# Optimization experiments

Hardware: AMD Instinct MI355X
Metric: run time of the kernel (lower is better)

Reference implementation:

```python
import jax, jax.numpy as jnp
import numpy as np

B_SZ = 2; L = 512; D_MODEL = 1024
D_STATE = 128; HEADDIM = 64; NGROUPS = 1
D_INNER = 2048; D_SSM = 2048
NHEADS = D_SSM // HEADDIM          # 32
HPG = NHEADS // NGROUPS            # heads per group
HALF = D_STATE // 2
D_IN_PROJ = D_INNER + D_SSM + 2 * NGROUPS * D_STATE + NHEADS + NHEADS + NHEADS * HALF  # 6464
EPS = 1e-5

def _rms(v, w):
    return v * jax.lax.rsqrt(jnp.mean(v * v, axis=-1, keepdims=True) + EPS) * w

def _rope(v, c, s):
    v1, v2 = v[..., :HALF], v[..., HALF:]
    return jnp.concatenate([v1 * c - v2 * s, v2 * c + v1 * s], axis=-1)

def setup_inputs() -> dict:
    key = jax.random.key(0)
    ks = jax.random.split(key, 3)
    rng = np.random.default_rng(0)
    # dt_bias init per module: inverse-softplus of dt ~ LogUniform(dt_min, dt_max)
    dt = np.exp(rng.random(NHEADS) * (np.log(0.1) - np.log(0.001)) + np.log(0.001))
    dt = np.maximum(dt, 1e-4)
    dt_bias = (dt + np.log(-np.expm1(-dt))).astype(np.float32)
    A_log = np.log(rng.uniform(1.0, 16.0, NHEADS)).astype(np.float32)
    return {
        'u': jax.random.normal(ks[0], (B_SZ, L, D_MODEL), jnp.float32),
        'W_in': jax.random.normal(ks[1], (D_MODEL, D_IN_PROJ), jnp.float32) / np.sqrt(D_MODEL),
        'W_out': jax.random.normal(ks[2], (D_INNER, D_MODEL), jnp.float32) / np.sqrt(D_INNER),
        'dt_bias': jnp.asarray(dt_bias),
        'A_log': jnp.asarray(A_log),
        'D': jnp.ones((NHEADS,), jnp.float32),
        'B_bias': jnp.ones((NGROUPS * D_STATE,), jnp.float32),
        'C_bias': jnp.ones((NGROUPS * D_STATE,), jnp.float32),
        'B_norm_w': jnp.ones((D_STATE,), jnp.float32),
        'C_norm_w': jnp.ones((D_STATE,), jnp.float32),
        'norm_w': jnp.ones((D_SSM,), jnp.float32),
    }

def reference(u, W_in, W_out, dt_bias, A_log, D, B_bias, C_bias, B_norm_w, C_norm_w, norm_w):
    b, l, _ = u.shape
    zxbcdt = u @ W_in  # (b, l, d_in_proj)
    s0 = D_INNER; s1 = s0 + D_SSM
    s2 = s1 + NGROUPS * D_STATE; s3 = s2 + NGROUPS * D_STATE
    s4 = s3 + NHEADS; s5 = s4 + NHEADS
    z = zxbcdt[..., :s0]
    x = zxbcdt[..., s0:s1]
    Bv = zxbcdt[..., s1:s2]
    Cv = zxbcdt[..., s2:s3]
    dt_raw = zxbcdt[..., s3:s4]
    lam_raw = zxbcdt[..., s4:s5]
    theta = zxbcdt[..., s5:]
    # BC bias + QK RMSNorm
    Bg = _rms((Bv + B_bias).reshape(b, l, NGROUPS, D_STATE), B_norm_w)
    Cg = _rms((Cv + C_bias).reshape(b, l, NGROUPS, D_STATE), C_norm_w)
    # data-dependent RoPE with cumulative angles, averaged over heads per group
    cum = jnp.cumsum(theta.reshape(b, l, NHEADS, HALF), axis=1)
    cos = jnp.cos(cum).reshape(b, l, NGROUPS, HPG, HALF).mean(3)
    sin = jnp.sin(cum).reshape(b, l, NGROUPS, HPG, HALF).mean(3)
    Bg = _rope(Bg, cos, sin)
    Cg = _rope(Cg, cos, sin)
    # discretization
    dt = jax.nn.softplus(dt_raw + dt_bias)          # (b, l, nheads)
    dA = jnp.exp(dt * (-jnp.exp(A_log)))            # (b, l, nheads)
    x = jax.nn.silu(x).reshape(b, l, NHEADS, HEADDIM)
    # trapezoidal blending of x and B with previous step
    lam = jax.nn.sigmoid(lam_raw)                   # (b, l, nheads)
    x_prev = jnp.pad(x[:, :-1], ((0, 0), (1, 0), (0, 0), (0, 0)))
    x_eff = lam[..., None] * x + (1.0 - lam[..., None]) * x_prev
    B_prev = jnp.pad(Bg[:, :-1], ((0, 0), (1, 0), (0, 0), (0, 0)))
    lam_g = lam.reshape(b, l, NGROUPS, HPG).mean(-1)[..., None]
    B_eff = lam_g * Bg + (1.0 - lam_g) * B_prev
    # selective scan over time
    xs = jnp.moveaxis(x_eff.reshape(b, l, NGROUPS, HPG, HEADDIM), 1, 0)
    dAs = jnp.moveaxis(dA.reshape(b, l, NGROUPS, HPG), 1, 0)
    dts = jnp.moveaxis(dt.reshape(b, l, NGROUPS, HPG), 1, 0)
    Bs = jnp.moveaxis(B_eff, 1, 0)
    Cs = jnp.moveaxis(Cg, 1, 0)
    def step(h, inp):
        dA_t, dt_t, x_t, B_t, C_t = inp
        # h: (b, g, hpg, headdim, d_state)
        h = dA_t[..., None, None] * h + (dt_t[..., None] * x_t)[..., None] * B_t[:, :, None, None, :]
        y_t = jnp.einsum('bgnpd,bgd->bgnp', h, C_t)
        return h, y_t
    h0 = jnp.zeros((b, NGROUPS, HPG, HEADDIM, D_STATE), u.dtype)
    _, ys = jax.lax.scan(step, h0, (dAs, dts, xs, Bs, Cs))
    y = jnp.moveaxis(ys, 0, 1).reshape(b, l, NHEADS, HEADDIM) + D[None, None, :, None] * x_eff
    # gated RMSNorm (norm after gate), then output projection
    y = y.reshape(b, l, D_SSM) * jax.nn.silu(z)
    y = y * jax.lax.rsqrt(jnp.mean(y * y, axis=-1, keepdims=True) + EPS) * norm_w
    return y @ W_out
```

## Files before the change

kernel.cpp:

```cpp
#include <hip/hip_runtime.h>
#include <hip/hip_bf16.h>
#include <cstdint>

#define TOK 1024
#define LSEQ 512
#define DMODEL 1024
#define DPROJ 6464
#define DPROJP 6528
#define DSSM 2048
#define NHEADS 32
#define HEADDIM 64
#define DSTATE 128
#define NCH 8
#define CL 64

typedef __attribute__((ext_vector_type(4))) float f32x4;
typedef _Float16 f16;
typedef __attribute__((ext_vector_type(8))) _Float16 f16x8;
typedef __attribute__((ext_vector_type(4))) _Float16 f16x4;
typedef __attribute__((ext_vector_type(8))) ushort u16x8;

__device__ __forceinline__ float silu_f(float x){
  return x*__builtin_amdgcn_rcpf(1.f+__expf(-x));
}

__device__ __forceinline__ void gload16(const void* g, void* l){
  __builtin_amdgcn_global_load_lds(
      (const __attribute__((address_space(1))) unsigned int*)g,
      (__attribute__((address_space(3))) unsigned int*)l, 16, 0, 0);
}

__global__ __launch_bounds__(256) void prep_kernel(
    const float* __restrict__ W_in, const float* __restrict__ W_out,
    const float* __restrict__ u,
    f16* __restrict__ WT, f16* __restrict__ WoT, f16* __restrict__ uhf)
{
  int b = blockIdx.x;
  if (b < 6528 + 2048){
    __shared__ float tile[32][33];
    const float* W; f16* T; int K, N, bx, by;
    if (b < 6528){ W = W_in;  T = WT;  K = DMODEL; N = DPROJ;  bx = b % 204;      by = b / 204; }
    else         { int ib = b - 6528; W = W_out; T = WoT; K = DSSM; N = DMODEL; bx = ib & 31; by = ib >> 5; }
    int tx = threadIdx.x & 31, ty = threadIdx.x >> 5;
    int n = bx*32 + tx;
    #pragma unroll
    for (int i=0;i<4;i++){
      int k = by*32 + ty + i*8;
      tile[ty+i*8][tx] = (n < N) ? W[(size_t)k*N + n] : 0.f;
    }
    __syncthreads();
    #pragma unroll
    for (int i=0;i<4;i++){
      int nn = bx*32 + ty + i*8;
      int kk = by*32 + tx;
      T[(size_t)nn*K + kk] = (f16)tile[tx][ty+i*8];
    }
  } else {
    int i = (b - 8576)*256 + threadIdx.x;
    f32x4 v = ((const f32x4*)u)[i];
    f16x4 h;
    #pragma unroll
    for (int j=0;j<4;j++) h[j] = (f16)v[j];
    *(f16x4*)&uhf[(size_t)i*4] = h;
  }
}

template<bool HOUT>
__global__ __launch_bounds__(512) void gemmh_kernel(
    const f16* __restrict__ A, const f16* __restrict__ B,
    void* __restrict__ Cv, int K, int kLen, int ldc, int nbn, int chunk)
{
  __shared__ ushort sA[2][8192], sB[2][8192];
  int bid = blockIdx.x;
  int newL = (bid & 7)*chunk + (bid >> 3);
  int bm = newL & 7;
  int pan = newL >> 3;
  int bn = pan % nbn;
  int z  = pan / nbn;
  int k0 = z * kLen;
  size_t zoff = (size_t)z * 1024 * ldc;

  int tid = threadIdx.x;
  int wid = tid >> 6, lane = tid & 63;
  int wr = wid >> 2, wc = wid & 3;
  int fr = lane & 15, kq = lane >> 4;
  f32x4 acc[4][2] = {};

  int srow = tid & 127;
  int skg  = (tid >> 7) & 3;
  const f16* gA = A + (size_t)(bm*128+srow)*K + k0 + skg*8;
  const f16* gB = B + (size_t)(bn*128+srow)*K + k0 + skg*8;

  int rA = kq*1024 + (wr*64 + fr)*8;
  int rB = kq*1024 + (wc*32 + fr)*8;
  int NK = kLen >> 6;

#define STAGE(buf, kk) { \
    const f16* pa = gA + (kk)*64; \
    const f16* pb = gB + (kk)*64; \
    gload16(pa,      &sA[buf][tid*8]); \
    gload16(pa + 32, &sA[buf][tid*8 + 4096]); \
    gload16(pb,      &sB[buf][tid*8]); \
    gload16(pb + 32, &sB[buf][tid*8 + 4096]); \
  }

  STAGE(0, 0)
  STAGE(1, 1)

  for (int ks=0; ks<NK; ks++){
    int cur = ks & 1;
    if (ks == NK-1) asm volatile("s_waitcnt vmcnt(0)" ::: "memory");
    else            asm volatile("s_waitcnt vmcnt(4)" ::: "memory");
    __builtin_amdgcn_s_barrier();
    f16x8 af0[4], af1[4], bf0[2], bf1[2];
    #pragma unroll
    for (int i=0;i<4;i++){
      af0[i] = *(const f16x8*)&sA[cur][rA + i*128];
      af1[i] = *(const f16x8*)&sA[cur][rA + 4096 + i*128];
    }
    #pragma unroll
    for (int j=0;j<2;j++){
      bf0[j] = *(const f16x8*)&sB[cur][rB + j*128];
      bf1[j] = *(const f16x8*)&sB[cur][rB + 4096 + j*128];
    }
    asm volatile("s_waitcnt lgkmcnt(0)" ::: "memory");
    __builtin_amdgcn_sched_barrier(0);
    __builtin_amdgcn_s_barrier();
    if (ks+2 < NK) STAGE(cur, ks+2)
    #pragma unroll
    for (int i=0;i<4;i++)
      #pragma unroll
      for (int j=0;j<2;j++)
        acc[i][j] = __builtin_amdgcn_mfma_f32_16x16x32_f16(af0[i], bf0[j], acc[i][j], 0,0,0);
    #pragma unroll
    for (int i=0;i<4;i++)
      #pragma unroll
      for (int j=0;j<2;j++)
        acc[i][j] = __builtin_amdgcn_mfma_f32_16x16x32_f16(af1[i], bf1[j], acc[i][j], 0,0,0);
  }
#undef STAGE
  int rq = kq * 4;
  #pragma unroll
  for (int i=0;i<4;i++){
    #pragma unroll
    for (int j=0;j<2;j++){
      int row = bm*128 + wr*64 + i*16 + rq;
      int col = bn*128 + wc*32 + j*16 + fr;
      #pragma unroll
      for (int q=0;q<4;q++){
        if constexpr (HOUT)
          ((f16*)Cv)[zoff + (size_t)(row+q)*ldc + col] = (f16)acc[i][j][q];
        else
          ((float*)Cv)[zoff + (size_t)(row+q)*ldc + col] = acc[i][j][q];
      }
    }
  }
}

__global__ __launch_bounds__(256) void red4_kernel(const f16* __restrict__ P, float* __restrict__ O){
  int i = blockIdx.x*256 + threadIdx.x;
  f16x4 a = ((const f16x4*)P)[i];
  f16x4 b = ((const f16x4*)P)[i + 262144];
  f16x4 c = ((const f16x4*)P)[i + 2*262144];
  f16x4 d = ((const f16x4*)P)[i + 3*262144];
  f32x4 v;
  #pragma unroll
  for (int j=0;j<4;j++) v[j] = (float)a[j] + (float)b[j] + (float)c[j] + (float)d[j];
  ((f32x4*)O)[i] = v;
}

__global__ __launch_bounds__(256) void thT_kernel(const float* __restrict__ zx,
    f16* __restrict__ thT)
{
  __shared__ float tile[64][65];
  int ci = blockIdx.x, li = blockIdx.y, bb = blockIdx.z;
  int tx = threadIdx.x & 63, ty = threadIdx.x >> 6;
  const float* src = zx + (size_t)(bb*LSEQ + li*64)*DPROJP + 4416 + ci*64;
  #pragma unroll
  for (int i=0;i<16;i++){
    int r = ty + i*4;
    tile[r][tx] = src[(size_t)r*DPROJP + tx];
  }
  __syncthreads();
  f16* dst = thT + ((size_t)bb*2048 + ci*64)*512 + (size_t)li*64;
  #pragma unroll
  for (int i=0;i<16;i++){
    int r = ty + i*4;
    dst[(size_t)r*512 + tx] = (f16)tile[tx][r];
  }
}

__global__ __launch_bounds__(512) void cum2_kernel(const f16* __restrict__ thT,
    float* __restrict__ cosm, float* __restrict__ sinm)
{
  __shared__ float wsum[8];
  int blk = blockIdx.x;
  int q = blk & 3, hd = (blk >> 2) & 63, b = blk >> 8;
  int l = threadIdx.x, lane = l & 63, w = l >> 6;
  float accc = 0.f, accs = 0.f;
  const f16* base = thT + (size_t)b*2048*512 + (size_t)(q*8)*64*512 + (size_t)hd*512;
  for (int h = 0; h < 8; h++){
    float x = (float)base[(size_t)h*64*512 + l];
    #pragma unroll
    for (int m=1; m<64; m<<=1){
      float v = __shfl_up(x, m, 64);
      if (lane >= m) x += v;
    }
    if (lane == 63) wsum[w] = x;
    __syncthreads();
    float pre = 0.f;
    for (int i=0;i<w;i++) pre += wsum[i];
    x += pre;
    float s, c;
    __sincosf(x, &s, &c);
    accc += c; accs += s;
    __syncthreads();
  }
  int t = b*LSEQ + l;
  cosm[q*TOK*64 + t*64+hd] = accc*(1.f/32.f);
  sinm[q*TOK*64 + t*64+hd] = accs*(1.f/32.f);
}

__global__ __launch_bounds__(256) void ew_kernel(const float* __restrict__ zx,
    const float* __restrict__ cosm, const float* __restrict__ sinm,
    const float* __restrict__ dt_bias, const float* __restrict__ A_log,
    const float* __restrict__ B_bias, const float* __restrict__ C_bias,
    const float* __restrict__ Bnw, const float* __restrict__ Cnw,
    f16* __restrict__ Bg, f16* __restrict__ Cg, float4* __restrict__ scal)
{
  int t = blockIdx.x; int tid = threadIdx.x;
  __shared__ float red[256];
  __shared__ float nb[128], nc[128];
  const float* row = zx + (size_t)t*DPROJP;
  float v;
  if (tid < 128) v = row[4096 + tid] + B_bias[tid];
  else           v = row[4224 + (tid-128)] + C_bias[tid-128];
  red[tid] = v*v;
  __syncthreads();
  #pragma unroll
  for (int s=64; s>0; s>>=1){
    if ((tid & 127) < s) red[tid] += red[tid + s];
    __syncthreads();
  }
  float ms = red[(tid < 128) ? 0 : 128] * (1.f/128.f);
  float rs = rsqrtf(ms + 1e-5f);
  float w  = (tid < 128) ? Bnw[tid] : Cnw[tid-128];
  float nv = v * rs * w;
  if (tid < 128) nb[tid] = nv; else nc[tid-128] = nv;
  __syncthreads();
  if (tid < 64){
    float c = cosm[t*64+tid] + cosm[TOK*64 + t*64+tid] + cosm[2*TOK*64 + t*64+tid] + cosm[3*TOK*64 + t*64+tid];
    float s = sinm[t*64+tid] + sinm[TOK*64 + t*64+tid] + sinm[2*TOK*64 + t*64+tid] + sinm[3*TOK*64 + t*64+tid];
    float a = nb[tid], bq = nb[tid+64];
    Bg[(size_t)t*128 + tid]      = (f16)(a*c - bq*s);
    Bg[(size_t)t*128 + 64 + tid] = (f16)(bq*c + a*s);
  } else if (tid < 128){
    int i = tid - 64;
    float c = cosm[t*64+i] + cosm[TOK*64 + t*64+i] + cosm[2*TOK*64 + t*64+i] + cosm[3*TOK*64 + t*64+i];
    float s = sinm[t*64+i] + sinm[TOK*64 + t*64+i] + sinm[2*TOK*64 + t*64+i] + sinm[3*TOK*64 + t*64+i];
    float a = nc[i], bq = nc[i+64];
    Cg[(size_t)t*128 + i]      = (f16)(a*c - bq*s);
    Cg[(size_t)t*128 + 64 + i] = (f16)(bq*c + a*s);
  } else if (tid < 160){
    int hh = tid - 128;
    float dtr = row[4352 + hh] + dt_bias[hh];
    float dtv = (dtr > 20.f) ? dtr : log1pf(expf(dtr));
    float dA  = expf(-dtv * expf(A_log[hh]));
    float lr  = row[4384 + hh];
    float lam = 1.f/(1.f + expf(-lr));
    float lg = lam;
    #pragma unroll
    for (int m=1;m<32;m<<=1) lg += __shfl_xor(lg, m, 64);
    lg *= (1.f/32.f);
    scal[(size_t)t*32 + hh] = make_float4(dtv, dA, lam, lg);
  }
}

#define CST 136
#define SST 72
__global__ __launch_bounds__(256, 2) void scanA_kernel(
    const float* __restrict__ zx, const f16* __restrict__ Bg,
    const f16* __restrict__ Cg, const float4* __restrict__ scal,
    const float* __restrict__ A_log, const float* __restrict__ Dp,
    f16* __restrict__ ypart, f16* __restrict__ hcarry,
    float* __restrict__ clog, float* __restrict__ AtotB)
{
  __shared__ __align__(16) f16 smC[64*CST];
  __shared__ __align__(16) f16 smB[64*CST];
  __shared__ __align__(16) f16 smBT[128*SST];
  __shared__ __align__(16) f16 smX[64*SST];
  __shared__ __align__(16) float sDt[64], sLam[64], sLg[64], sCl[64], sW[64];
  f16* sSp = smC;

  int blk = blockIdx.x;
  int c = blk & 7, h = (blk>>3)&31, b = blk>>8;
  int idx = blk;
  int t0 = b*LSEQ + c*CL;
  int tid = threadIdx.x;
  int w = tid >> 6, lane = tid & 63;
  int fr = lane & 15, kq = lane >> 4;

  {
    int s = tid >> 2, dq4 = (tid & 3) * 32;
    const ushort* src = (const ushort*)(Cg + (size_t)(t0+s)*128 + dq4);
    ushort* dst = (ushort*)(smC + s*CST + dq4);
    #pragma unroll
    for (int i=0;i<4;i++) *(u16x8*)(dst + i*8) = *(const u16x8*)(src + i*8);
  }
  if (tid < 64){
    float4 sc = scal[(size_t)(t0+tid)*32 + h];
    float a  = __expf(A_log[h]);
    float cl = -sc.x * a * 1.44269504088896f;
    #pragma unroll
    for (int m=1; m<64; m<<=1){
      float v = __shfl_up(cl, m, 64);
      if (lane >= m) cl += v;
    }
    float cl63 = __shfl(cl, 63, 64);
    sDt[tid] = sc.x; sLam[tid] = sc.z; sLg[tid] = sc.w;
    sCl[tid] = cl;
    sW[tid]  = exp2f(cl63 - cl) * sc.x;
    clog[(size_t)idx*64 + tid] = cl;
    if (tid == 63) AtotB[idx] = exp2f(cl63);
  }
  __syncthreads();

  {
    int s = tid >> 2, dq4 = (tid & 3) * 32;
    float lg = sLg[s], wgt = sW[s];
    bool zp = (s == 0 && c == 0);
    const f16* bc_p = Bg + (size_t)(t0+s)*128 + dq4;
    const f16* bp_p = Bg + (size_t)(t0+s-1)*128 + dq4;
    #pragma unroll
    for (int i=0;i<32;i+=4){
      f16x4 bc4 = *(const f16x4*)(bc_p + i);
      f16x4 bp4 = {0,0,0,0};
      if (!zp) bp4 = *(const f16x4*)(bp_p + i);
      f16x4 be4;
      #pragma unroll
      for (int e=0;e<4;e++){
        float bc = (float)bc4[e], bp = (float)bp4[e];
        float be = bp + lg*(bc - bp);
        be4[e] = (f16)be;
        smBT[(dq4+i+e)*SST + s] = (f16)(be * wgt);
      }
      *(f16x4*)(smB + s*CST + dq4 + i) = be4;
    }
  }
  {
    int p = tid & 63, sg = tid >> 6;
    int s0 = sg*16;
    const float* xbase = zx + 2048 + h*64 + p;
    float xp_ = 0.f;
    if (!(s0 == 0 && c == 0))
      xp_ = silu_f(xbase[(size_t)(t0+s0-1)*DPROJP]);
    #pragma unroll
    for (int i=0;i<16;i++){
      int s = s0 + i;
      float xs = silu_f(xbase[(size_t)(t0+s)*DPROJP]);
      smX[p*SST + s] = (f16)(xp_ + sLam[s]*(xs - xp_));
      xp_ = xs;
    }
  }
  __syncthreads();

  int tq = w >> 1, sq = w & 1;
  f32x4 acc1[2][2] = {};
  #pragma unroll
  for (int kt=0; kt<4; kt++){
    f16x8 ah[2], bh[2];
    #pragma unroll
    for (int i=0;i<2;i++)
      ah[i] = *(const f16x8*)&smC[(tq*32 + i*16 + fr)*CST + kt*32 + kq*8];
    #pragma unroll
    for (int j=0;j<2;j++)
      bh[j] = *(const f16x8*)&smB[(sq*32 + j*16 + fr)*CST + kt*32 + kq*8];
    #pragma unroll
    for (int i=0;i<2;i++)
      #pragma unroll
      for (int j=0;j<2;j++)
        acc1[i][j] = __builtin_amdgcn_mfma_f32_16x16x32_f16(ah[i], bh[j], acc1[i][j], 0,0,0);
  }
  #pragma unroll
  for (int i=0;i<2;i++){
    int tb = tq*32 + i*16 + kq*4;
    f32x4 clt = *(const f32x4*)&sCl[tb];
    #pragma unroll
    for (int j=0;j<2;j++){
      int scol = sq*32 + j*16 + fr;
      float cls = sCl[scol], dts = sDt[scol];
      #pragma unroll
      for (int q=0;q<4;q++){
        float m = (tb+q >= scol) ? exp2f(clt[q]-cls)*dts : 0.f;
        acc1[i][j][q] *= m;
      }
    }
  }
  __syncthreads();
  #pragma unroll
  for (int i=0;i<2;i++){
    int tb = tq*32 + i*16 + kq*4;
    #pragma unroll
    for (int j=0;j<2;j++){
      int scol = sq*32 + j*16 + fr;
      #pragma unroll
      for (int q=0;q<4;q++)
        sSp[(tb+q)*SST + scol] = (f16)acc1[i][j][q];
    }
  }
  __syncthreads();

  float Dh = Dp[h];
  {
    f32x4 acc2[2][2] = {};
    #pragma unroll
    for (int kt=0; kt<2; kt++){
      f16x8 ah[2], bh[2];
      #pragma unroll
      for (int i=0;i<2;i++)
        ah[i] = *(const f16x8*)&sSp[(tq*32 + i*16 + fr)*SST + kt*32 + kq*8];
      #pragma unroll
      for (int j=0;j<2;j++)
        bh[j] = *(const f16x8*)&smX[(sq*32 + j*16 + fr)*SST + kt*32 + kq*8];
      #pragma unroll
      for (int i=0;i<2;i++)
        #pragma unroll
        for (int j=0;j<2;j++)
          acc2[i][j] = __builtin_amdgcn_mfma_f32_16x16x32_f16(ah[i], bh[j], acc2[i][j], 0,0,0);
    }
    #pragma unroll
    for (int i=0;i<2;i++){
      int tb = tq*32 + i*16 + kq*4;
      #pragma unroll
      for (int j=0;j<2;j++){
        int pc = sq*32 + j*16 + fr;
        #pragma unroll
        for (int q=0;q<4;q++){
          float y = acc2[i][j][q] + Dh * (float)smX[pc*SST + tb + q];
          ypart[(size_t)(t0+tb+q)*DSSM + h*64 + pc] = (f16)y;
        }
      }
    }
  }

  {
    f32x4 acc4[2][4] = {};
    int ph = w >> 1, dh = w & 1;
    #pragma unroll
    for (int kt=0; kt<2; kt++){
      f16x8 ah[2], bh[4];
      #pragma unroll
      for (int i=0;i<2;i++)
        ah[i] = *(const f16x8*)&smX[(ph*32 + i*16 + fr)*SST + kt*32 + kq*8];
      #pragma unroll
      for (int j=0;j<4;j++)
        bh[j] = *(const f16x8*)&smBT[(dh*64 + j*16 + fr)*SST + kt*32 + kq*8];
      #pragma unroll
      for (int i=0;i<2;i++)
        #pragma unroll
        for (int j=0;j<4;j++)
          acc4[i][j] = __builtin_amdgcn_mfma_f32_16x16x32_f16(ah[i], bh[j], acc4[i][j], 0,0,0);
    }
    size_t hb = (size_t)idx * 64 * 128;
    #pragma unroll
    for (int i=0;i<2;i++){
      int pb = ph*32 + i*16 + kq*4;
      #pragma unroll
      for (int j=0;j<4;j++){
        int dc = dh*64 + j*16 + fr;
        #pragma unroll
        for (int q=0;q<4;q++)
          hcarry[hb + (size_t)(pb+q)*128 + dc] = (f16)acc4[i][j][q];
      }
    }
  }
}

__global__ __launch_bounds__(256) void scan2_kernel(f16* __restrict__ hcarry,
    const float* __restrict__ AtotB)
{
  int idx = blockIdx.x*256 + threadIdx.x;
  int d = idx & 127, pp = (idx >> 7) & 63, h = (idx >> 13) & 31, b = idx >> 18;
  size_t base = ((size_t)(b*32+h)*512 + pp)*128 + d;
  float Hin = 0.f;
  #pragma unroll
  for (int c=0; c<NCH; c++){
    float Atot = AtotB[(b*32+h)*8 + c];
    float S = (float)hcarry[base + (size_t)c*8192];
    hcarry[base + (size_t)c*8192] = (f16)Hin;
    Hin = Atot*Hin + S;
  }
}

__global__ __launch_bounds__(256) void scanB_kernel(
    const f16* __restrict__ Cg, const f16* __restrict__ hcarry,
    const float* __restrict__ clog, f16* __restrict__ ypart)
{
  __shared__ __align__(16) f16 smC[64*CST];
  __shared__ __align__(16) f16 smH[64*CST];
  __shared__ __align__(16) float sK[64];
  int blk = blockIdx.x;
  int c = blk & 7, h = (blk>>3)&31, b = blk>>8;
  int idx = blk;
  int t0 = b*LSEQ + c*CL;
  int tid = threadIdx.x;
  int w = tid >> 6, lane = tid & 63;
  int fr = lane & 15, kq = lane >> 4;
  {
    int s = tid >> 2, dq4 = (tid & 3) * 32;
    const ushort* src = (const ushort*)(Cg + (size_t)(t0+s)*128 + dq4);
    ushort* dst = (ushort*)(smC + s*CST + dq4);
    #pragma unroll
    for (int i=0;i<4;i++) *(u16x8*)(dst + i*8) = *(const u16x8*)(src + i*8);
    const ushort* hs = (const ushort*)(hcarry + (size_t)idx*8192 + (size_t)s*128 + dq4);
    ushort* hd = (ushort*)(smH + s*CST + dq4);
    #pragma unroll
    for (int i=0;i<4;i++) *(u16x8*)(hd + i*8) = *(const u16x8*)(hs + i*8);
  }
  if (tid < 64) sK[tid] = exp2f(clog[(size_t)idx*64 + tid]);
  __syncthreads();

  int tq = w >> 1, pq = w & 1;
  f32x4 acc[2][2] = {};
  #pragma unroll
  for (int kt=0; kt<4; kt++){
    f16x8 ah[2], bh[2];
    #pragma unroll
    for (int i=0;i<2;i++)
      ah[i] = *(const f16x8*)&smC[(tq*32 + i*16 + fr)*CST + kt*32 + kq*8];
    #pragma unroll
    for (int j=0;j<2;j++)
      bh[j] = *(const f16x8*)&smH[(pq*32 + j*16 + fr)*CST + kt*32 + kq*8];
    #pragma unroll
    for (int i=0;i<2;i++)
      #pragma unroll
      for (int j=0;j<2;j++)
        acc[i][j] = __builtin_amdgcn_mfma_f32_16x16x32_f16(ah[i], bh[j], acc[i][j], 0,0,0);
  }
  #pragma unroll
  for (int i=0;i<2;i++){
    int tb = tq*32 + i*16 + kq*4;
    f32x4 kv = *(const f32x4*)&sK[tb];
    #pragma unroll
    for (int j=0;j<2;j++){
      int pc = pq*32 + j*16 + fr;
      #pragma unroll
      for (int q=0;q<4;q++)
        ypart[(size_t)TOK*DSSM + (size_t)(t0+tb+q)*DSSM + h*64 + pc] = (f16)(acc[i][j][q]*kv[q]);
    }
  }
}

__global__ __launch_bounds__(256) void fin_kernel(const float* __restrict__ zx,
    const f16* __restrict__ ypart, const float* __restrict__ normw,
    f16* __restrict__ yf)
{
  int t = blockIdx.x; int tid = threadIdx.x;
  __shared__ float red[256];
  float vloc[8];
  float ss = 0.f;
  #pragma unroll
  for (int i=0;i<8;i++){
    int cc = tid + i*256;
    float y = (float)ypart[(size_t)t*DSSM + cc]
            + (float)ypart[(size_t)(TOK + t)*DSSM + cc];
    float z = zx[(size_t)t*DPROJP + cc];
    float v = y * (z / (1.f + expf(-z)));
    vloc[i] = v; ss += v*v;
  }
  red[tid] = ss; __syncthreads();
  #pragma unroll
  for (int s=128; s>0; s>>=1){ if (tid < s) red[tid] += red[tid+s]; __syncthreads(); }
  float rs = rsqrtf(red[0]*(1.f/2048.f) + 1e-5f);
  #pragma unroll
  for (int i=0;i<8;i++){
    int cc = tid + i*256;
    yf[(size_t)t*DSSM + cc] = (f16)(vloc[i]*rs*normw[cc]);
  }
}

extern "C" void kernel_launch(void* const* d_in, const int* in_sizes, int n_in,
                              void* d_out, int out_size, void* d_ws, size_t ws_size,
                              hipStream_t stream)
{
  const float* u      = (const float*)d_in[0];
  const float* W_in   = (const float*)d_in[1];
  const float* W_out  = (const float*)d_in[2];
  const float* dt_bias= (const float*)d_in[3];
  const float* A_log  = (const float*)d_in[4];
  const float* Dp     = (const float*)d_in[5];
  const float* B_bias = (const float*)d_in[6];
  const float* C_bias = (const float*)d_in[7];
  const float* Bnw    = (const float*)d_in[8];
  const float* Cnw    = (const float*)d_in[9];
  const float* normw  = (const float*)d_in[10];
  float* out = (float*)d_out;

  char* ws = (char*)d_ws;
  size_t o = 0;
  auto alloc = [&](size_t bytes)->char*{
    char* r = ws + o; o = (o + bytes + 255) & ~(size_t)255; return r;
  };
  f16*  WT   = (f16*)alloc((size_t)DPROJP*DMODEL*2);
  f16*  WoT  = (f16*)alloc((size_t)DMODEL*DSSM*2);
  f16*  uhf  = (f16*)alloc((size_t)TOK*DMODEL*2);
  f16*  yf   = (f16*)alloc((size_t)TOK*DSSM*2);
  float*  zx   = (float*)alloc((size_t)TOK*DPROJP*4);
  f16*   thT  = (f16*)alloc((size_t)2*2048*512*2);
  float*  cosm = (float*)alloc((size_t)4*TOK*64*4);
  float*  sinm = (float*)alloc((size_t)4*TOK*64*4);
  f16*   Bgb  = (f16*)alloc((size_t)TOK*128*2);
  f16*   Cgb  = (f16*)alloc((size_t)TOK*128*2);
  float4* scal = (float4*)alloc((size_t)TOK*32*16);
  f16*   ypart= (f16*)alloc((size_t)2*TOK*DSSM*2);
  f16*   hcarry=(f16*)alloc((size_t)2*32*NCH*64*128*2);
  float*  clog = (float*)alloc((size_t)512*64*4);
  float*  AtotB= (float*)alloc((size_t)512*4);
  f16*   Cpart =(f16*)alloc((size_t)4*TOK*DMODEL*2);

  prep_kernel<<<dim3(9600), dim3(256), 0, stream>>>(W_in, W_out, u, WT, WoT, uhf);

  gemmh_kernel<false><<<dim3(408), dim3(512), 0, stream>>>(uhf, WT, zx, DMODEL, DMODEL, DPROJP, 51, 51);

  thT_kernel<<<dim3(32, 8, 2), dim3(256), 0, stream>>>(zx, thT);
  cum2_kernel<<<dim3(512), dim3(512), 0, stream>>>(thT, cosm, sinm);

  ew_kernel<<<dim3(TOK), dim3(256), 0, stream>>>(zx, cosm, sinm, dt_bias, A_log,
                                                 B_bias, C_bias, Bnw, Cnw, Bgb, Cgb, scal);

  scanA_kernel<<<dim3(512),  dim3(256), 0, stream>>>(zx, Bgb, Cgb, scal, A_log, Dp,
                                                     ypart, hcarry, clog, AtotB);
  scan2_kernel<<<dim3(2048), dim3(256), 0, stream>>>(hcarry, AtotB);
  scanB_kernel<<<dim3(512),  dim3(256), 0, stream>>>(Cgb, hcarry, clog, ypart);

  fin_kernel<<<dim3(TOK), dim3(256), 0, stream>>>(zx, ypart, normw, yf);

  gemmh_kernel<true><<<dim3(256), dim3(512), 0, stream>>>(yf, WoT, Cpart, DSSM, 512, DMODEL, 8, 32);
  red4_kernel<<<dim3(TOK*DMODEL/1024), dim3(256), 0, stream>>>(Cpart, out);
}
```

Measured before the change: 115.4 us.

## Store in-projection output as fp16 and fuse theta transpose into GEMM epilogue

The in-projection GEMM now writes its output as fp16 instead of fp32, which halves that buffer's write and later read traffic. Its epilogue also writes the theta columns straight into the transposed thT buffer, so the separate thT transpose kernel is gone. The dt columns are kept in fp32 in a small side buffer, because softplus and the decay exponent are sensitive to them. The transposed epilogue stores are strided and poorly coalesced, and z, x, B, C and lambda now carry fp16 rounding error.

```diff
diff --git a/kernel.cpp b/kernel.cpp
--- a/kernel.cpp
+++ b/kernel.cpp
@@ -65,10 +65,11 @@
   }
 }
 
-template<bool HOUT>
+template<int MODE>
 __global__ __launch_bounds__(512) void gemmh_kernel(
     const f16* __restrict__ A, const f16* __restrict__ B,
-    void* __restrict__ Cv, int K, int kLen, int ldc, int nbn, int chunk)
+    f16* __restrict__ C, float* __restrict__ dtb, f16* __restrict__ thT,
+    int K, int kLen, int ldc, int nbn, int chunk)
 {
   __shared__ ushort sA[2][8192], sB[2][8192];
   int bid = blockIdx.x;
@@ -148,10 +149,20 @@
       int col = bn*128 + wc*32 + j*16 + fr;
       #pragma unroll
       for (int q=0;q<4;q++){
-        if constexpr (HOUT)
-          ((f16*)Cv)[zoff + (size_t)(row+q)*ldc + col] = (f16)acc[i][j][q];
-        else
-          ((float*)Cv)[zoff + (size_t)(row+q)*ldc + col] = acc[i][j][q];
+        float av = acc[i][j][q];
+        f16 hv = (f16)av;
+        if constexpr (MODE == 0){
+          int r = row + q;
+          C[(size_t)r*ldc + col] = hv;
+          if (col >= 4352 && col < 4384)
+            dtb[r*32 + (col - 4352)] = av;
+          if (col >= 4416 && col < 4416 + 2048){
+            int bb = r >> 9, l = r & 511;
+            thT[((size_t)(bb*2048 + (col - 4416)))*512 + l] = hv;
+          }
+        } else {
+          C[zoff + (size_t)(row+q)*ldc + col] = hv;
+        }
       }
     }
   }
@@ -167,27 +178,6 @@
   #pragma unroll
   for (int j=0;j<4;j++) v[j] = (float)a[j] + (float)b[j] + (float)c[j] + (float)d[j];
   ((f32x4*)O)[i] = v;
-}
-
-__global__ __launch_bounds__(256) void thT_kernel(const float* __restrict__ zx,
-    f16* __restrict__ thT)
-{
-  __shared__ float tile[64][65];
-  int ci = blockIdx.x, li = blockIdx.y, bb = blockIdx.z;
-  int tx = threadIdx.x & 63, ty = threadIdx.x >> 6;
-  const float* src = zx + (size_t)(bb*LSEQ + li*64)*DPROJP + 4416 + ci*64;
-  #pragma unroll
-  for (int i=0;i<16;i++){
-    int r = ty + i*4;
-    tile[r][tx] = src[(size_t)r*DPROJP + tx];
-  }
-  __syncthreads();
-  f16* dst = thT + ((size_t)bb*2048 + ci*64)*512 + (size_t)li*64;
-  #pragma unroll
-  for (int i=0;i<16;i++){
-    int r = ty + i*4;
-    dst[(size_t)r*512 + tx] = (f16)tile[tx][r];
-  }
 }
 
 __global__ __launch_bounds__(512) void cum2_kernel(const f16* __restrict__ thT,
@@ -221,7 +211,8 @@
   sinm[q*TOK*64 + t*64+hd] = accs*(1.f/32.f);
 }
 
-__global__ __launch_bounds__(256) void ew_kernel(const float* __restrict__ zx,
+__global__ __launch_bounds__(256) void ew_kernel(const f16* __restrict__ zxh,
+    const float* __restrict__ dtb,
     const float* __restrict__ cosm, const float* __restrict__ sinm,
     const float* __restrict__ dt_bias, const float* __restrict__ A_log,
     const float* __restrict__ B_bias, const float* __restrict__ C_bias,
@@ -231,10 +222,10 @@
   int t = blockIdx.x; int tid = threadIdx.x;
   __shared__ float red[256];
   __shared__ float nb[128], nc[128];
-  const float* row = zx + (size_t)t*DPROJP;
+  const f16* row = zxh + (size_t)t*DPROJP;
   float v;
-  if (tid < 128) v = row[4096 + tid] + B_bias[tid];
-  else           v = row[4224 + (tid-128)] + C_bias[tid-128];
+  if (tid < 128) v = (float)row[4096 + tid] + B_bias[tid];
+  else           v = (float)row[4224 + (tid-128)] + C_bias[tid-128];
   red[tid] = v*v;
   __syncthreads();
   #pragma unroll
@@ -263,10 +254,10 @@
     Cg[(size_t)t*128 + 64 + i] = (f16)(bq*c + a*s);
   } else if (tid < 160){
     int hh = tid - 128;
-    float dtr = row[4352 + hh] + dt_bias[hh];
+    float dtr = dtb[t*32 + hh] + dt_bias[hh];
     float dtv = (dtr > 20.f) ? dtr : log1pf(expf(dtr));
     float dA  = expf(-dtv * expf(A_log[hh]));
-    float lr  = row[4384 + hh];
+    float lr  = (float)row[4384 + hh];
     float lam = 1.f/(1.f + expf(-lr));
     float lg = lam;
     #pragma unroll
@@ -279,7 +270,7 @@
 #define CST 136
 #define SST 72
 __global__ __launch_bounds__(256, 2) void scanA_kernel(
-    const float* __restrict__ zx, const f16* __restrict__ Bg,
+    const f16* __restrict__ zxh, const f16* __restrict__ Bg,
     const f16* __restrict__ Cg, const float4* __restrict__ scal,
     const float* __restrict__ A_log, const float* __restrict__ Dp,
     f16* __restrict__ ypart, f16* __restrict__ hcarry,
@@ -350,14 +341,14 @@
   {
     int p = tid & 63, sg = tid >> 6;
     int s0 = sg*16;
-    const float* xbase = zx + 2048 + h*64 + p;
+    const f16* xbase = zxh + 2048 + h*64 + p;
     float xp_ = 0.f;
     if (!(s0 == 0 && c == 0))
-      xp_ = silu_f(xbase[(size_t)(t0+s0-1)*DPROJP]);
+      xp_ = silu_f((float)xbase[(size_t)(t0+s0-1)*DPROJP]);
     #pragma unroll
     for (int i=0;i<16;i++){
       int s = s0 + i;
-      float xs = silu_f(xbase[(size_t)(t0+s)*DPROJP]);
+      float xs = silu_f((float)xbase[(size_t)(t0+s)*DPROJP]);
       smX[p*SST + s] = (f16)(xp_ + sLam[s]*(xs - xp_));
       xp_ = xs;
     }
@@ -551,7 +542,7 @@
   }
 }
 
-__global__ __launch_bounds__(256) void fin_kernel(const float* __restrict__ zx,
+__global__ __launch_bounds__(256) void fin_kernel(const f16* __restrict__ zxh,
     const f16* __restrict__ ypart, const float* __restrict__ normw,
     f16* __restrict__ yf)
 {
@@ -564,7 +555,7 @@
     int cc = tid + i*256;
     float y = (float)ypart[(size_t)t*DSSM + cc]
             + (float)ypart[(size_t)(TOK + t)*DSSM + cc];
-    float z = zx[(size_t)t*DPROJP + cc];
+    float z = (float)zxh[(size_t)t*DPROJP + cc];
     float v = y * (z / (1.f + expf(-z)));
     vloc[i] = v; ss += v*v;
   }
@@ -605,7 +596,8 @@
   f16*  WoT  = (f16*)alloc((size_t)DMODEL*DSSM*2);
   f16*  uhf  = (f16*)alloc((size_t)TOK*DMODEL*2);
   f16*  yf   = (f16*)alloc((size_t)TOK*DSSM*2);
-  float*  zx   = (float*)alloc((size_t)TOK*DPROJP*4);
+  f16*  zxh  = (f16*)alloc((size_t)TOK*DPROJP*2);
+  float* dtb = (float*)alloc((size_t)TOK*32*4);
   f16*   thT  = (f16*)alloc((size_t)2*2048*512*2);
   float*  cosm = (float*)alloc((size_t)4*TOK*64*4);
   float*  sinm = (float*)alloc((size_t)4*TOK*64*4);
@@ -620,21 +612,20 @@
 
   prep_kernel<<<dim3(9600), dim3(256), 0, stream>>>(W_in, W_out, u, WT, WoT, uhf);
 
-  gemmh_kernel<false><<<dim3(408), dim3(512), 0, stream>>>(uhf, WT, zx, DMODEL, DMODEL, DPROJP, 51, 51);
-
-  thT_kernel<<<dim3(32, 8, 2), dim3(256), 0, stream>>>(zx, thT);
+  gemmh_kernel<0><<<dim3(408), dim3(512), 0, stream>>>(uhf, WT, zxh, dtb, thT, DMODEL, DMODEL, DPROJP, 51, 51);
+
   cum2_kernel<<<dim3(512), dim3(512), 0, stream>>>(thT, cosm, sinm);
 
-  ew_kernel<<<dim3(TOK), dim3(256), 0, stream>>>(zx, cosm, sinm, dt_bias, A_log,
+  ew_kernel<<<dim3(TOK), dim3(256), 0, stream>>>(zxh, dtb, cosm, sinm, dt_bias, A_log,
                                                  B_bias, C_bias, Bnw, Cnw, Bgb, Cgb, scal);
 
-  scanA_kernel<<<dim3(512),  dim3(256), 0, stream>>>(zx, Bgb, Cgb, scal, A_log, Dp,
+  scanA_kernel<<<dim3(512),  dim3(256), 0, stream>>>(zxh, Bgb, Cgb, scal, A_log, Dp,
                                                      ypart, hcarry, clog, AtotB);
   scan2_kernel<<<dim3(2048), dim3(256), 0, stream>>>(hcarry, AtotB);
   scanB_kernel<<<dim3(512),  dim3(256), 0, stream>>>(Cgb, hcarry, clog, ypart);
 
-  fin_kernel<<<dim3(TOK), dim3(256), 0, stream>>>(zx, ypart, normw, yf);
-
-  gemmh_kernel<true><<<dim3(256), dim3(512), 0, stream>>>(yf, WoT, Cpart, DSSM, 512, DMODEL, 8, 32);
+  fin_kernel<<<dim3(TOK), dim3(256), 0, stream>>>(zxh, ypart, normw, yf);
+
+  gemmh_kernel<1><<<dim3(256), dim3(512), 0, stream>>>(yf, WoT, Cpart, nullptr, nullptr, DSSM, 512, DMODEL, 8, 32);
   red4_kernel<<<dim3(TOK*DMODEL/1024), dim3(256), 0, stream>>>(Cpart, out);
 }
```

Measured after the change: 123.8 us. 7.3% more time.
